# Optimization experiments

Measured on AMD Instinct MI355X. Metric: run time of the kernel, lower is better.

The kernel has to match this reference:

```python
import jax, jax.numpy as jnp
import numpy as np

EMBED_DIM = 512
NUM_HEADS = 8
HEAD_DIM = EMBED_DIM // NUM_HEADS


def setup_inputs() -> dict:
    key = jax.random.key(0)
    ks = jax.random.split(key, 9)
    d = EMBED_DIM
    s = 1.0 / np.sqrt(d)
    inp = {
        "x": jax.random.normal(ks[0], (2, 4096, d), dtype=jnp.float32),
        # torch nn.Linear weights are [out, in]; we store them the same way
        "Wq": jax.random.uniform(ks[1], (d, d), jnp.float32, -s, s),
        "bq": jax.random.uniform(ks[2], (d,), jnp.float32, -s, s),
        "Wk": jax.random.uniform(ks[3], (d, d), jnp.float32, -s, s),
        "bk": jax.random.uniform(ks[4], (d,), jnp.float32, -s, s),
        "Wv": jax.random.uniform(ks[5], (d, d), jnp.float32, -s, s),
        "bv": jax.random.uniform(ks[6], (d,), jnp.float32, -s, s),
        "Wo": jax.random.uniform(ks[7], (d, d), jnp.float32, -s, s),
        "bo": jax.random.uniform(ks[8], (d,), jnp.float32, -s, s),
    }
    return inp


def reference(x, Wq, bq, Wk, bk, Wv, bv, Wo, bo):
    B, S, D = x.shape
    H, Hd = NUM_HEADS, HEAD_DIM

    def proj(W, b):  # torch Linear: x @ W.T + b
        y = jnp.einsum("bsd,ed->bse", x, W) + b
        return y.reshape(B, S, H, Hd).transpose(0, 2, 1, 3)  # [B,H,S,Hd]

    Q = proj(Wq, bq)
    K = proj(Wk, bk)
    V = proj(Wv, bv)

    scale = 1.0 / jnp.sqrt(jnp.float32(Hd))
    scores = jnp.einsum("bhqd,bhkd->bhqk", Q, K) * scale  # [B,H,S,S]
    attn = jax.nn.softmax(scores, axis=-1)
    out = jnp.einsum("bhqk,bhkd->bhqd", attn, V)  # [B,H,S,Hd]
    out = out.transpose(0, 2, 1, 3).reshape(B, S, D)
    return jnp.einsum("bsd,ed->bse", out, Wo) + bo
```

## Files before the change

### kernel.cpp

```cpp
#include <hip/hip_runtime.h>


typedef unsigned short ushortT;
typedef __attribute__((ext_vector_type(8))) short short8;
typedef __attribute__((ext_vector_type(4))) float f32x4;
typedef __attribute__((ext_vector_type(16))) float f32x16;
typedef __attribute__((ext_vector_type(4))) unsigned int uint4v;
typedef __attribute__((ext_vector_type(2))) unsigned int uint2v;

__device__ __forceinline__ ushortT f2bf(float f) {
    unsigned int u = __builtin_bit_cast(unsigned int, f);
    u += 0x7FFFu + ((u >> 16) & 1u);
    return (ushortT)(u >> 16);
}

__device__ __forceinline__ unsigned int cvtpk(float lo, float hi) {
    unsigned int d;
    asm("v_cvt_pk_bf16_f32 %0, %1, %2" : "=v"(d) : "v"(lo), "v"(hi));
    return d;
}

__device__ __forceinline__ uint4v pk8(f32x4 a0, f32x4 a1) {
    uint4v r = { cvtpk(a0[0], a0[1]), cvtpk(a0[2], a0[3]),
                 cvtpk(a1[0], a1[1]), cvtpk(a1[2], a1[3]) };
    return r;
}

__device__ __forceinline__ void plswap(unsigned int &a, unsigned int &b) {
    uint2v r = __builtin_amdgcn_permlane32_swap(a, b, false, false);
    a = r[0]; b = r[1];
}

#define GLDA 40
#define ALDK 72

__global__ __launch_bounds__(256) void proj_qkv(
    const float* __restrict__ x,
    const float* __restrict__ Wq, const float* __restrict__ bq,
    const float* __restrict__ Wk, const float* __restrict__ bk,
    const float* __restrict__ Wv, const float* __restrict__ bv,
    ushortT* __restrict__ Qw, ushortT* __restrict__ Kw,
    ushortT* __restrict__ Vtw, float qscale)
{
    __shared__ __align__(16) ushortT As[128 * GLDA];
    __shared__ __align__(16) ushortT Bs[128 * GLDA];
    const int t = threadIdx.x;
    const int w = t >> 6, lane = t & 63;
    const int quad = lane >> 4, l15 = lane & 15;
    const int z = blockIdx.z;
    const int bx = blockIdx.x, by = blockIdx.y;
    const int wm = (w >> 1) * 64, wn = (w & 1) * 64;

    const float* W    = (z == 0) ? Wq : (z == 1) ? Wk : Wv;
    const float* bias = (z == 0) ? bq : (z == 1) ? bk : bv;
    const float* Asrc = (z < 2) ? x : W;
    const float* Bsrc = (z < 2) ? W : x;
    const int arow0 = (z < 2) ? bx * 128 : by * 128;
    const int brow0 = (z < 2) ? by * 128 : bx * 128;

    const int sr0 = t >> 2, sc0 = (t & 3) * 8;
    const int sr1 = (t + 256) >> 2, sc1 = ((t + 256) & 3) * 8;

    f32x4 pa[2][2], pb[2][2];
    {
        const float* ap0 = Asrc + (size_t)(arow0 + sr0) * 512 + sc0;
        const float* ap1 = Asrc + (size_t)(arow0 + sr1) * 512 + sc1;
        const float* bp0 = Bsrc + (size_t)(brow0 + sr0) * 512 + sc0;
        const float* bp1 = Bsrc + (size_t)(brow0 + sr1) * 512 + sc1;
        pa[0][0] = *(const f32x4*)ap0; pa[0][1] = *(const f32x4*)(ap0 + 4);
        pa[1][0] = *(const f32x4*)ap1; pa[1][1] = *(const f32x4*)(ap1 + 4);
        pb[0][0] = *(const f32x4*)bp0; pb[0][1] = *(const f32x4*)(bp0 + 4);
        pb[1][0] = *(const f32x4*)bp1; pb[1][1] = *(const f32x4*)(bp1 + 4);
    }

    f32x4 acc[4][4] = {};

    for (int k0 = 0; k0 < 512; k0 += 32) {
        *(uint4v*)(As + sr0 * GLDA + sc0) = pk8(pa[0][0], pa[0][1]);
        *(uint4v*)(As + sr1 * GLDA + sc1) = pk8(pa[1][0], pa[1][1]);
        *(uint4v*)(Bs + sr0 * GLDA + sc0) = pk8(pb[0][0], pb[0][1]);
        *(uint4v*)(Bs + sr1 * GLDA + sc1) = pk8(pb[1][0], pb[1][1]);
        __syncthreads();

        if (k0 < 480) {
            const int kn = k0 + 32;
            const float* ap0 = Asrc + (size_t)(arow0 + sr0) * 512 + kn + sc0;
            const float* ap1 = Asrc + (size_t)(arow0 + sr1) * 512 + kn + sc1;
            const float* bp0 = Bsrc + (size_t)(brow0 + sr0) * 512 + kn + sc0;
            const float* bp1 = Bsrc + (size_t)(brow0 + sr1) * 512 + kn + sc1;
            pa[0][0] = *(const f32x4*)ap0; pa[0][1] = *(const f32x4*)(ap0 + 4);
            pa[1][0] = *(const f32x4*)ap1; pa[1][1] = *(const f32x4*)(ap1 + 4);
            pb[0][0] = *(const f32x4*)bp0; pb[0][1] = *(const f32x4*)(bp0 + 4);
            pb[1][0] = *(const f32x4*)bp1; pb[1][1] = *(const f32x4*)(bp1 + 4);
        }

        short8 af[4], bfr[4];
#pragma unroll
        for (int i = 0; i < 4; i++)
            af[i] = *(const short8*)(As + (wm + i * 16 + l15) * GLDA + quad * 8);
#pragma unroll
        for (int i = 0; i < 4; i++)
            bfr[i] = *(const short8*)(Bs + (wn + i * 16 + l15) * GLDA + quad * 8);
#pragma unroll
        for (int mi = 0; mi < 4; mi++)
#pragma unroll
            for (int ni = 0; ni < 4; ni++)
                acc[mi][ni] = __builtin_amdgcn_mfma_f32_16x16x32_bf16(
                    af[mi], bfr[ni], acc[mi][ni], 0, 0, 0);
        __syncthreads();
    }

    if (z < 2) {
        ushortT* Y = (z == 0) ? Qw : Kw;
        const float sc = (z == 0) ? qscale : 1.0f;
#pragma unroll
        for (int ni = 0; ni < 4; ni++) {
            int col = brow0 + wn + ni * 16 + l15;
            float bv_ = bias[col];
#pragma unroll
            for (int mi = 0; mi < 4; mi++)
#pragma unroll
                for (int r = 0; r < 4; r++) {
                    int row = arow0 + wm + mi * 16 + quad * 4 + r;
                    Y[(size_t)row * 512 + col] = f2bf((acc[mi][ni][r] + bv_) * sc);
                }
        }
    } else {
        const int bidx = brow0 >> 12;
        const int s0 = brow0 & 4095;
#pragma unroll
        for (int mi = 0; mi < 4; mi++)
#pragma unroll
            for (int r = 0; r < 4; r++) {
                int ch = arow0 + wm + mi * 16 + quad * 4 + r;
                float bv_ = bias[ch];
#pragma unroll
                for (int ni = 0; ni < 4; ni++) {
                    int s = s0 + wn + ni * 16 + l15;
                    Vtw[(size_t)bidx * 2097152 + (size_t)ch * 4096 + s] =
                        f2bf(acc[mi][ni][r] + bv_);
                }
            }
    }
}

__global__ __launch_bounds__(256) void gemm_out(
    const ushortT* __restrict__ X, const float* __restrict__ W,
    const float* __restrict__ bias, float* __restrict__ Y)
{
    __shared__ __align__(16) ushortT As[128 * GLDA];
    __shared__ __align__(16) ushortT Bs[128 * GLDA];
    const int t = threadIdx.x;
    const int w = t >> 6, lane = t & 63;
    const int quad = lane >> 4, l15 = lane & 15;
    const int bm = blockIdx.x * 128, bn = blockIdx.y * 128;
    const int wm = (w >> 1) * 64, wn = (w & 1) * 64;

    const int sr0 = t >> 2, sc0 = (t & 3) * 8;
    const int sr1 = (t + 256) >> 2, sc1 = ((t + 256) & 3) * 8;

    uint4v pa[2];
    f32x4 pb[2][2];
    {
        pa[0] = *(const uint4v*)(X + (size_t)(bm + sr0) * 512 + sc0);
        pa[1] = *(const uint4v*)(X + (size_t)(bm + sr1) * 512 + sc1);
        const float* bp0 = W + (size_t)(bn + sr0) * 512 + sc0;
        const float* bp1 = W + (size_t)(bn + sr1) * 512 + sc1;
        pb[0][0] = *(const f32x4*)bp0; pb[0][1] = *(const f32x4*)(bp0 + 4);
        pb[1][0] = *(const f32x4*)bp1; pb[1][1] = *(const f32x4*)(bp1 + 4);
    }

    f32x4 acc[4][4] = {};

    for (int k0 = 0; k0 < 512; k0 += 32) {
        *(uint4v*)(As + sr0 * GLDA + sc0) = pa[0];
        *(uint4v*)(As + sr1 * GLDA + sc1) = pa[1];
        *(uint4v*)(Bs + sr0 * GLDA + sc0) = pk8(pb[0][0], pb[0][1]);
        *(uint4v*)(Bs + sr1 * GLDA + sc1) = pk8(pb[1][0], pb[1][1]);
        __syncthreads();

        if (k0 < 480) {
            const int kn = k0 + 32;
            pa[0] = *(const uint4v*)(X + (size_t)(bm + sr0) * 512 + kn + sc0);
            pa[1] = *(const uint4v*)(X + (size_t)(bm + sr1) * 512 + kn + sc1);
            const float* bp0 = W + (size_t)(bn + sr0) * 512 + kn + sc0;
            const float* bp1 = W + (size_t)(bn + sr1) * 512 + kn + sc1;
            pb[0][0] = *(const f32x4*)bp0; pb[0][1] = *(const f32x4*)(bp0 + 4);
            pb[1][0] = *(const f32x4*)bp1; pb[1][1] = *(const f32x4*)(bp1 + 4);
        }

        short8 af[4], bfr[4];
#pragma unroll
        for (int i = 0; i < 4; i++)
            af[i] = *(const short8*)(As + (wm + i * 16 + l15) * GLDA + quad * 8);
#pragma unroll
        for (int i = 0; i < 4; i++)
            bfr[i] = *(const short8*)(Bs + (wn + i * 16 + l15) * GLDA + quad * 8);
#pragma unroll
        for (int mi = 0; mi < 4; mi++)
#pragma unroll
            for (int ni = 0; ni < 4; ni++)
                acc[mi][ni] = __builtin_amdgcn_mfma_f32_16x16x32_bf16(
                    af[mi], bfr[ni], acc[mi][ni], 0, 0, 0);
        __syncthreads();
    }

#pragma unroll
    for (int ni = 0; ni < 4; ni++) {
        int col = bn + wn + ni * 16 + l15;
        float bv = bias[col];
#pragma unroll
        for (int mi = 0; mi < 4; mi++)
#pragma unroll
            for (int r = 0; r < 4; r++) {
                int row = bm + wm + mi * 16 + quad * 4 + r;
                Y[(size_t)row * 512 + col] = acc[mi][ni][r] + bv;
            }
    }
}

__device__ __forceinline__ void softmax_pack(const f32x16 &sacc, float &lp,
                                             uint4v &B0, uint4v &B1)
{
    float p[16];
#pragma unroll
    for (int r = 0; r < 16; r++) {
        p[r] = __builtin_amdgcn_exp2f(sacc[r]);
        lp += p[r];
    }
    unsigned int c00 = cvtpk(p[0],  p[1]),  c01 = cvtpk(p[2],  p[3]);
    unsigned int c10 = cvtpk(p[4],  p[5]),  c11 = cvtpk(p[6],  p[7]);
    unsigned int c20 = cvtpk(p[8],  p[9]),  c21 = cvtpk(p[10], p[11]);
    unsigned int c30 = cvtpk(p[12], p[13]), c31 = cvtpk(p[14], p[15]);
    plswap(c00, c10);
    plswap(c01, c11);
    plswap(c20, c30);
    plswap(c21, c31);
    B0 = uint4v{ c00, c01, c10, c11 };
    B1 = uint4v{ c20, c21, c30, c31 };
}

__global__ __launch_bounds__(512, 2) void attn(
    const ushortT* Q, const ushortT* __restrict__ K,
    const ushortT* __restrict__ Vt, ushortT* O)
{
    __shared__ __align__(16) ushortT SM[2][2][2][64 * ALDK];

    const int t = threadIdx.x;
    const int w = t >> 6, lane = t & 63;
    const int half = w >> 2, qw = w & 3;
    const int l31 = lane & 31, hh = lane >> 5;
    const int qt = blockIdx.x, bh = blockIdx.y;
    const int b = bh >> 3, h = bh & 7;
    const size_t qbase = (size_t)b * 4096 + qt * 256 + qw * 64;

    short8 qf[2][4];
#pragma unroll
    for (int qg = 0; qg < 2; qg++) {
        const ushortT* qp = Q + (qbase + qg * 32 + l31) * 512 + h * 64 + hh * 8;
#pragma unroll
        for (int dk = 0; dk < 4; dk++)
            qf[qg][dk] = *(const short8*)(qp + dk * 16);
    }

    f32x16 oacc[2][2] = {};
    float lpart[2] = {};

    const int kofs = half * 2048;
    const ushortT* Kbase = K + ((size_t)b * 4096 + kofs) * 512 + h * 64;
    const ushortT* Vbase = Vt + (size_t)b * 2097152 + (size_t)h * 64 * 4096 + kofs;

    const int th = t & 255;
    const int srow = th >> 3, scol = (th & 7) * 8;
    uint4v kg[2], vg[2];

#pragma unroll
    for (int i = 0; i < 2; i++) {
        kg[i] = *(const uint4v*)(Kbase + (size_t)(srow + 32 * i) * 512 + scol);
        vg[i] = *(const uint4v*)(Vbase + (size_t)(srow + 32 * i) * 4096 + scol);
    }
#pragma unroll
    for (int i = 0; i < 2; i++) {
        *(uint4v*)(SM[0][half][0] + (srow + 32 * i) * ALDK + scol) = kg[i];
        *(uint4v*)(SM[1][half][0] + (srow + 32 * i) * ALDK + scol) = vg[i];
    }
    __syncthreads();

    for (int kt = 0; kt < 32; kt++) {
        const int cur = kt & 1;

        if (kt < 31) {
            const int kb = (kt + 1) * 64;
#pragma unroll
            for (int i = 0; i < 2; i++) {
                kg[i] = *(const uint4v*)(Kbase + (size_t)(kb + srow + 32 * i) * 512 + scol);
                vg[i] = *(const uint4v*)(Vbase + (size_t)(srow + 32 * i) * 4096 + kb + scol);
            }
        }

        const ushortT* Kt  = SM[0][half][cur];
        const ushortT* Vtl = SM[1][half][cur];

#pragma unroll
        for (int st = 0; st < 2; st++) {
            short8 kf[4];
#pragma unroll
            for (int dk = 0; dk < 4; dk++)
                kf[dk] = *(const short8*)(Kt + (st * 32 + l31) * ALDK + dk * 16 + hh * 8);
            f32x16 s0 = {}, s1 = {};
#pragma unroll
            for (int dk = 0; dk < 4; dk++) {
                s0 = __builtin_amdgcn_mfma_f32_32x32x16_bf16(kf[dk], qf[0][dk], s0, 0, 0, 0);
                s1 = __builtin_amdgcn_mfma_f32_32x32x16_bf16(kf[dk], qf[1][dk], s1, 0, 0, 0);
            }

            uint4v B00, B01, B10, B11;
            softmax_pack(s0, lpart[0], B00, B01);
            softmax_pack(s1, lpart[1], B10, B11);
            short8 p00 = __builtin_bit_cast(short8, B00);
            short8 p01 = __builtin_bit_cast(short8, B01);
            short8 p10 = __builtin_bit_cast(short8, B10);
            short8 p11 = __builtin_bit_cast(short8, B11);

#pragma unroll
            for (int dt = 0; dt < 2; dt++) {
                short8 vf0 = *(const short8*)(Vtl + (dt * 32 + l31) * ALDK + st * 32 + hh * 8);
                short8 vf1 = *(const short8*)(Vtl + (dt * 32 + l31) * ALDK + st * 32 + 16 + hh * 8);
                oacc[0][dt] = __builtin_amdgcn_mfma_f32_32x32x16_bf16(vf0, p00, oacc[0][dt], 0, 0, 0);
                oacc[0][dt] = __builtin_amdgcn_mfma_f32_32x32x16_bf16(vf1, p01, oacc[0][dt], 0, 0, 0);
                oacc[1][dt] = __builtin_amdgcn_mfma_f32_32x32x16_bf16(vf0, p10, oacc[1][dt], 0, 0, 0);
                oacc[1][dt] = __builtin_amdgcn_mfma_f32_32x32x16_bf16(vf1, p11, oacc[1][dt], 0, 0, 0);
            }
        }

        if (kt < 31) {
            const int nb = cur ^ 1;
#pragma unroll
            for (int i = 0; i < 2; i++) {
                *(uint4v*)(SM[0][half][nb] + (srow + 32 * i) * ALDK + scol) = kg[i];
                *(uint4v*)(SM[1][half][nb] + (srow + 32 * i) * ALDK + scol) = vg[i];
            }
        }
        __syncthreads();
    }

    float* scratch = (float*)&SM[0][0][0][0];
    float* prow = scratch + (size_t)(qw * 64 + lane) * 68;

    if (half == 1) {
#pragma unroll
        for (int qg = 0; qg < 2; qg++)
#pragma unroll
            for (int dt = 0; dt < 2; dt++)
#pragma unroll
                for (int m = 0; m < 4; m++) {
                    f32x4 v4 = { oacc[qg][dt][4 * m + 0], oacc[qg][dt][4 * m + 1],
                                 oacc[qg][dt][4 * m + 2], oacc[qg][dt][4 * m + 3] };
                    *(f32x4*)(prow + qg * 32 + dt * 16 + m * 4) = v4;
                }
        prow[64] = lpart[0];
        prow[65] = lpart[1];
    }
    __syncthreads();

    if (half == 0) {
#pragma unroll
        for (int qg = 0; qg < 2; qg++) {
            float sum = lpart[qg] + prow[64 + qg];
            float l = sum + __shfl_xor(sum, 32);
            float rl = 1.0f / l;

            ushortT* orow = O + (qbase + qg * 32 + l31) * 512 + h * 64 + hh * 4;
#pragma unroll
            for (int dt = 0; dt < 2; dt++)
#pragma unroll
                for (int m = 0; m < 4; m++) {
                    f32x4 v4 = *(const f32x4*)(prow + qg * 32 + dt * 16 + m * 4);
                    unsigned int u0 = cvtpk((oacc[qg][dt][4 * m + 0] + v4[0]) * rl,
                                            (oacc[qg][dt][4 * m + 1] + v4[1]) * rl);
                    unsigned int u1 = cvtpk((oacc[qg][dt][4 * m + 2] + v4[2]) * rl,
                                            (oacc[qg][dt][4 * m + 3] + v4[3]) * rl);
                    uint2v st2 = { u0, u1 };
                    *(uint2v*)(orow + dt * 32 + m * 8) = st2;
                }
        }
    }
}

extern "C" void kernel_launch(void* const* d_in, const int* in_sizes, int n_in,
                              void* d_out, int out_size, void* d_ws, size_t ws_size,
                              hipStream_t stream)
{
    const float* x  = (const float*)d_in[0];
    const float* Wq = (const float*)d_in[1];
    const float* bq = (const float*)d_in[2];
    const float* Wk = (const float*)d_in[3];
    const float* bk = (const float*)d_in[4];
    const float* Wv = (const float*)d_in[5];
    const float* bv = (const float*)d_in[6];
    const float* Wo = (const float*)d_in[7];
    const float* bo = (const float*)d_in[8];

    ushortT* ws  = (ushortT*)d_ws;
    ushortT* Qw  = ws;
    ushortT* Kw  = ws + 4194304;
    ushortT* Vtw = ws + 2 * 4194304;

    const float qscale = 0.125f * 1.44269504089f;

    proj_qkv<<<dim3(64, 4, 3), 256, 0, stream>>>(
        x, Wq, bq, Wk, bk, Wv, bv, Qw, Kw, Vtw, qscale);
    attn<<<dim3(16, 16), 512, 0, stream>>>(Qw, Kw, Vtw, Qw);
    gemm_out<<<dim3(64, 4), 256, 0, stream>>>(Qw, Wo, bo, (float*)d_out);
}
```

Baseline: 189.6 us.

## Use 512-thread blocks and K-tile 64 in projection GEMMs

```diff
diff --git a/kernel.cpp b/kernel.cpp
--- a/kernel.cpp
+++ b/kernel.cpp
@@ -26,15 +26,21 @@
     return r;
 }
 
+__device__ __forceinline__ uint4v ldpk8(const float* p) {
+    f32x4 a0 = *(const f32x4*)p;
+    f32x4 a1 = *(const f32x4*)(p + 4);
+    return pk8(a0, a1);
+}
+
 __device__ __forceinline__ void plswap(unsigned int &a, unsigned int &b) {
     uint2v r = __builtin_amdgcn_permlane32_swap(a, b, false, false);
     a = r[0]; b = r[1];
 }
 
-#define GLDA 40
+#define GLDB 72
 #define ALDK 72
 
-__global__ __launch_bounds__(256) void proj_qkv(
+__global__ __launch_bounds__(512, 4) void proj_qkv(
     const float* __restrict__ x,
     const float* __restrict__ Wq, const float* __restrict__ bq,
     const float* __restrict__ Wk, const float* __restrict__ bk,
@@ -42,14 +48,14 @@
     ushortT* __restrict__ Qw, ushortT* __restrict__ Kw,
     ushortT* __restrict__ Vtw, float qscale)
 {
-    __shared__ __align__(16) ushortT As[128 * GLDA];
-    __shared__ __align__(16) ushortT Bs[128 * GLDA];
+    __shared__ __align__(16) ushortT As[128 * GLDB];
+    __shared__ __align__(16) ushortT Bs[128 * GLDB];
     const int t = threadIdx.x;
     const int w = t >> 6, lane = t & 63;
     const int quad = lane >> 4, l15 = lane & 15;
     const int z = blockIdx.z;
     const int bx = blockIdx.x, by = blockIdx.y;
-    const int wm = (w >> 1) * 64, wn = (w & 1) * 64;
+    const int wm = (w >> 1) * 32, wn = (w & 1) * 64;
 
     const float* W    = (z == 0) ? Wq : (z == 1) ? Wk : Wv;
     const float* bias = (z == 0) ? bq : (z == 1) ? bk : bv;
@@ -58,55 +64,47 @@
     const int arow0 = (z < 2) ? bx * 128 : by * 128;
     const int brow0 = (z < 2) ? by * 128 : bx * 128;
 
-    const int sr0 = t >> 2, sc0 = (t & 3) * 8;
-    const int sr1 = (t + 256) >> 2, sc1 = ((t + 256) & 3) * 8;
-
-    f32x4 pa[2][2], pb[2][2];
-    {
-        const float* ap0 = Asrc + (size_t)(arow0 + sr0) * 512 + sc0;
-        const float* ap1 = Asrc + (size_t)(arow0 + sr1) * 512 + sc1;
-        const float* bp0 = Bsrc + (size_t)(brow0 + sr0) * 512 + sc0;
-        const float* bp1 = Bsrc + (size_t)(brow0 + sr1) * 512 + sc1;
-        pa[0][0] = *(const f32x4*)ap0; pa[0][1] = *(const f32x4*)(ap0 + 4);
-        pa[1][0] = *(const f32x4*)ap1; pa[1][1] = *(const f32x4*)(ap1 + 4);
-        pb[0][0] = *(const f32x4*)bp0; pb[0][1] = *(const f32x4*)(bp0 + 4);
-        pb[1][0] = *(const f32x4*)bp1; pb[1][1] = *(const f32x4*)(bp1 + 4);
-    }
-
-    f32x4 acc[4][4] = {};
-
-    for (int k0 = 0; k0 < 512; k0 += 32) {
-        *(uint4v*)(As + sr0 * GLDA + sc0) = pk8(pa[0][0], pa[0][1]);
-        *(uint4v*)(As + sr1 * GLDA + sc1) = pk8(pa[1][0], pa[1][1]);
-        *(uint4v*)(Bs + sr0 * GLDA + sc0) = pk8(pb[0][0], pb[0][1]);
-        *(uint4v*)(Bs + sr1 * GLDA + sc1) = pk8(pb[1][0], pb[1][1]);
+    const int sr0 = t >> 3, sc0 = (t & 7) * 8;
+
+    uint4v pka[2], pkb[2];
+    pka[0] = ldpk8(Asrc + (size_t)(arow0 + sr0) * 512 + sc0);
+    pka[1] = ldpk8(Asrc + (size_t)(arow0 + sr0 + 64) * 512 + sc0);
+    pkb[0] = ldpk8(Bsrc + (size_t)(brow0 + sr0) * 512 + sc0);
+    pkb[1] = ldpk8(Bsrc + (size_t)(brow0 + sr0 + 64) * 512 + sc0);
+
+    f32x4 acc[2][4] = {};
+
+    for (int k0 = 0; k0 < 512; k0 += 64) {
+        *(uint4v*)(As + sr0 * GLDB + sc0) = pka[0];
+        *(uint4v*)(As + (sr0 + 64) * GLDB + sc0) = pka[1];
+        *(uint4v*)(Bs + sr0 * GLDB + sc0) = pkb[0];
+        *(uint4v*)(Bs + (sr0 + 64) * GLDB + sc0) = pkb[1];
         __syncthreads();
 
-        if (k0 < 480) {
-            const int kn = k0 + 32;
-            const float* ap0 = Asrc + (size_t)(arow0 + sr0) * 512 + kn + sc0;
-            const float* ap1 = Asrc + (size_t)(arow0 + sr1) * 512 + kn + sc1;
-            const float* bp0 = Bsrc + (size_t)(brow0 + sr0) * 512 + kn + sc0;
-            const float* bp1 = Bsrc + (size_t)(brow0 + sr1) * 512 + kn + sc1;
-            pa[0][0] = *(const f32x4*)ap0; pa[0][1] = *(const f32x4*)(ap0 + 4);
-            pa[1][0] = *(const f32x4*)ap1; pa[1][1] = *(const f32x4*)(ap1 + 4);
-            pb[0][0] = *(const f32x4*)bp0; pb[0][1] = *(const f32x4*)(bp0 + 4);
-            pb[1][0] = *(const f32x4*)bp1; pb[1][1] = *(const f32x4*)(bp1 + 4);
-        }
-
-        short8 af[4], bfr[4];
-#pragma unroll
-        for (int i = 0; i < 4; i++)
-            af[i] = *(const short8*)(As + (wm + i * 16 + l15) * GLDA + quad * 8);
-#pragma unroll
-        for (int i = 0; i < 4; i++)
-            bfr[i] = *(const short8*)(Bs + (wn + i * 16 + l15) * GLDA + quad * 8);
-#pragma unroll
-        for (int mi = 0; mi < 4; mi++)
-#pragma unroll
-            for (int ni = 0; ni < 4; ni++)
-                acc[mi][ni] = __builtin_amdgcn_mfma_f32_16x16x32_bf16(
-                    af[mi], bfr[ni], acc[mi][ni], 0, 0, 0);
+        if (k0 < 448) {
+            const int kn = k0 + 64;
+            pka[0] = ldpk8(Asrc + (size_t)(arow0 + sr0) * 512 + kn + sc0);
+            pka[1] = ldpk8(Asrc + (size_t)(arow0 + sr0 + 64) * 512 + kn + sc0);
+            pkb[0] = ldpk8(Bsrc + (size_t)(brow0 + sr0) * 512 + kn + sc0);
+            pkb[1] = ldpk8(Bsrc + (size_t)(brow0 + sr0 + 64) * 512 + kn + sc0);
+        }
+
+#pragma unroll
+        for (int kk = 0; kk < 2; kk++) {
+            short8 af[2], bfr[4];
+#pragma unroll
+            for (int i = 0; i < 2; i++)
+                af[i] = *(const short8*)(As + (wm + i * 16 + l15) * GLDB + kk * 32 + quad * 8);
+#pragma unroll
+            for (int i = 0; i < 4; i++)
+                bfr[i] = *(const short8*)(Bs + (wn + i * 16 + l15) * GLDB + kk * 32 + quad * 8);
+#pragma unroll
+            for (int mi = 0; mi < 2; mi++)
+#pragma unroll
+                for (int ni = 0; ni < 4; ni++)
+                    acc[mi][ni] = __builtin_amdgcn_mfma_f32_16x16x32_bf16(
+                        af[mi], bfr[ni], acc[mi][ni], 0, 0, 0);
+        }
         __syncthreads();
     }
 
@@ -118,7 +116,7 @@
             int col = brow0 + wn + ni * 16 + l15;
             float bv_ = bias[col];
 #pragma unroll
-            for (int mi = 0; mi < 4; mi++)
+            for (int mi = 0; mi < 2; mi++)
 #pragma unroll
                 for (int r = 0; r < 4; r++) {
                     int row = arow0 + wm + mi * 16 + quad * 4 + r;
@@ -129,7 +127,7 @@
         const int bidx = brow0 >> 12;
         const int s0 = brow0 & 4095;
 #pragma unroll
-        for (int mi = 0; mi < 4; mi++)
+        for (int mi = 0; mi < 2; mi++)
 #pragma unroll
             for (int r = 0; r < 4; r++) {
                 int ch = arow0 + wm + mi * 16 + quad * 4 + r;
@@ -144,64 +142,59 @@
     }
 }
 
-__global__ __launch_bounds__(256) void gemm_out(
+__global__ __launch_bounds__(512, 4) void gemm_out(
     const ushortT* __restrict__ X, const float* __restrict__ W,
     const float* __restrict__ bias, float* __restrict__ Y)
 {
-    __shared__ __align__(16) ushortT As[128 * GLDA];
-    __shared__ __align__(16) ushortT Bs[128 * GLDA];
+    __shared__ __align__(16) ushortT As[128 * GLDB];
+    __shared__ __align__(16) ushortT Bs[128 * GLDB];
     const int t = threadIdx.x;
     const int w = t >> 6, lane = t & 63;
     const int quad = lane >> 4, l15 = lane & 15;
     const int bm = blockIdx.x * 128, bn = blockIdx.y * 128;
-    const int wm = (w >> 1) * 64, wn = (w & 1) * 64;
-
-    const int sr0 = t >> 2, sc0 = (t & 3) * 8;
-    const int sr1 = (t + 256) >> 2, sc1 = ((t + 256) & 3) * 8;
-
-    uint4v pa[2];
-    f32x4 pb[2][2];
-    {
-        pa[0] = *(const uint4v*)(X + (size_t)(bm + sr0) * 512 + sc0);
-        pa[1] = *(const uint4v*)(X + (size_t)(bm + sr1) * 512 + sc1);
-        const float* bp0 = W + (size_t)(bn + sr0) * 512 + sc0;
-        const float* bp1 = W + (size_t)(bn + sr1) * 512 + sc1;
-        pb[0][0] = *(const f32x4*)bp0; pb[0][1] = *(const f32x4*)(bp0 + 4);
-        pb[1][0] = *(const f32x4*)bp1; pb[1][1] = *(const f32x4*)(bp1 + 4);
-    }
-
-    f32x4 acc[4][4] = {};
-
-    for (int k0 = 0; k0 < 512; k0 += 32) {
-        *(uint4v*)(As + sr0 * GLDA + sc0) = pa[0];
-        *(uint4v*)(As + sr1 * GLDA + sc1) = pa[1];
-        *(uint4v*)(Bs + sr0 * GLDA + sc0) = pk8(pb[0][0], pb[0][1]);
-        *(uint4v*)(Bs + sr1 * GLDA + sc1) = pk8(pb[1][0], pb[1][1]);
+    const int wm = (w >> 1) * 32, wn = (w & 1) * 64;
+
+    const int sr0 = t >> 3, sc0 = (t & 7) * 8;
+
+    uint4v pa[2], pkb[2];
+    pa[0] = *(const uint4v*)(X + (size_t)(bm + sr0) * 512 + sc0);
+    pa[1] = *(const uint4v*)(X + (size_t)(bm + sr0 + 64) * 512 + sc0);
+    pkb[0] = ldpk8(W + (size_t)(bn + sr0) * 512 + sc0);
+    pkb[1] = ldpk8(W + (size_t)(bn + sr0 + 64) * 512 + sc0);
+
+    f32x4 acc[2][4] = {};
+
+    for (int k0 = 0; k0 < 512; k0 += 64) {
+        *(uint4v*)(As + sr0 * GLDB + sc0) = pa[0];
+        *(uint4v*)(As + (sr0 + 64) * GLDB + sc0) = pa[1];
+        *(uint4v*)(Bs + sr0 * GLDB + sc0) = pkb[0];
+        *(uint4v*)(Bs + (sr0 + 64) * GLDB + sc0) = pkb[1];
         __syncthreads();
 
-        if (k0 < 480) {
-            const int kn = k0 + 32;
+        if (k0 < 448) {
+            const int kn = k0 + 64;
             pa[0] = *(const uint4v*)(X + (size_t)(bm + sr0) * 512 + kn + sc0);
-            pa[1] = *(const uint4v*)(X + (size_t)(bm + sr1) * 512 + kn + sc1);
-            const float* bp0 = W + (size_t)(bn + sr0) * 512 + kn + sc0;
-            const float* bp1 = W + (size_t)(bn + sr1) * 512 + kn + sc1;
-            pb[0][0] = *(const f32x4*)bp0; pb[0][1] = *(const f32x4*)(bp0 + 4);
-            pb[1][0] = *(const f32x4*)bp1; pb[1][1] = *(const f32x4*)(bp1 + 4);
-        }
-
-        short8 af[4], bfr[4];
-#pragma unroll
-        for (int i = 0; i < 4; i++)
-            af[i] = *(const short8*)(As + (wm + i * 16 + l15) * GLDA + quad * 8);
-#pragma unroll
-        for (int i = 0; i < 4; i++)
-            bfr[i] = *(const short8*)(Bs + (wn + i * 16 + l15) * GLDA + quad * 8);
-#pragma unroll
-        for (int mi = 0; mi < 4; mi++)
-#pragma unroll
-            for (int ni = 0; ni < 4; ni++)
-                acc[mi][ni] = __builtin_amdgcn_mfma_f32_16x16x32_bf16(
-                    af[mi], bfr[ni], acc[mi][ni], 0, 0, 0);
+            pa[1] = *(const uint4v*)(X + (size_t)(bm + sr0 + 64) * 512 + kn + sc0);
+            pkb[0] = ldpk8(W + (size_t)(bn + sr0) * 512 + kn + sc0);
+            pkb[1] = ldpk8(W + (size_t)(bn + sr0 + 64) * 512 + kn + sc0);
+        }
+
+#pragma unroll
+        for (int kk = 0; kk < 2; kk++) {
+            short8 af[2], bfr[4];
+#pragma unroll
+            for (int i = 0; i < 2; i++)
+                af[i] = *(const short8*)(As + (wm + i * 16 + l15) * GLDB + kk * 32 + quad * 8);
+#pragma unroll
+            for (int i = 0; i < 4; i++)
+                bfr[i] = *(const short8*)(Bs + (wn + i * 16 + l15) * GLDB + kk * 32 + quad * 8);
+#pragma unroll
+            for (int mi = 0; mi < 2; mi++)
+#pragma unroll
+                for (int ni = 0; ni < 4; ni++)
+                    acc[mi][ni] = __builtin_amdgcn_mfma_f32_16x16x32_bf16(
+                        af[mi], bfr[ni], acc[mi][ni], 0, 0, 0);
+        }
         __syncthreads();
     }
 
@@ -210,7 +203,7 @@
         int col = bn + wn + ni * 16 + l15;
         float bv = bias[col];
 #pragma unroll
-        for (int mi = 0; mi < 4; mi++)
+        for (int mi = 0; mi < 2; mi++)
 #pragma unroll
             for (int r = 0; r < 4; r++) {
                 int row = bm + wm + mi * 16 + quad * 4 + r;
@@ -408,8 +401,8 @@
 
     const float qscale = 0.125f * 1.44269504089f;
 
-    proj_qkv<<<dim3(64, 4, 3), 256, 0, stream>>>(
+    proj_qkv<<<dim3(64, 4, 3), 512, 0, stream>>>(
         x, Wq, bq, Wk, bk, Wv, bv, Qw, Kw, Vtw, qscale);
     attn<<<dim3(16, 16), 512, 0, stream>>>(Qw, Kw, Vtw, Qw);
-    gemm_out<<<dim3(64, 4), 256, 0, stream>>>(Qw, Wo, bo, (float*)d_out);
-}
+    gemm_out<<<dim3(64, 4), 512, 0, stream>>>(Qw, Wo, bo, (float*)d_out);
+}
```

Result: slower. 196.6 us (+3.7%).
